# Kernel tuning notes

Hardware: AMD Instinct MI355X
Metric: run time of the kernel (lower is better)

## Reference

```python
import jax, jax.numpy as jnp
from jax import lax
import numpy as np

B, N = 64, 8192


def setup_inputs() -> dict:
    key = jax.random.key(0)
    ks = jax.random.split(key, 8)
    v = jax.random.normal(ks[0], (B, N), jnp.float32)
    mask = (jax.random.uniform(ks[1], (B, N)) > 0.5).astype(jnp.float32)
    def init_w(k, shape, fan_in):
        return (jax.random.normal(k, shape, jnp.float32) / np.float32(np.sqrt(fan_in)))
    # Conv1d weights: (out_ch, in_ch, kernel)
    w1 = init_w(ks[2], (32, 2, 5), 2 * 5)
    b1 = jnp.zeros((32,), jnp.float32)
    w2 = init_w(ks[3], (32, 32, 5), 32 * 5)
    b2 = jnp.zeros((32,), jnp.float32)
    w3 = init_w(ks[4], (2, 32, 5), 32 * 5)
    b3 = jnp.zeros((2,), jnp.float32)
    return dict(v=v, mask=mask, w1=w1, b1=b1, w2=w2, b2=b2, w3=w3, b3=b3)


def _bk_gii(he_diag):
    """Diagonal of G = (zI - H)^{-1} for tridiagonal H (diag=he_diag, sub=super=1), z=1j.
    Uses the standard left/right continued-fraction recursions:
      L_0 = z - a_0,   L_i = z - a_i - 1/L_{i-1}
      R_{N-1} = z - a_{N-1},   R_i = z - a_i - 1/R_{i+1}
      G_ii = 1 / (L_i + R_i - (z - a_i))
    Returns (B, N, 2) features = [Re G_ii, Im G_ii]."""
    z = jnp.complex64(1j)
    a = he_diag.astype(jnp.complex64).T  # (N, B)

    def step(carry, a_i):
        nxt = z - a_i - 1.0 / carry
        return nxt, nxt

    L0 = z - a[0]
    _, Ls = lax.scan(step, L0, a[1:])
    L = jnp.concatenate([L0[None], Ls], axis=0)  # (N, B)

    Rl = z - a[-1]
    _, Rs = lax.scan(step, Rl, a[:-1][::-1])
    R = jnp.concatenate([Rl[None], Rs], axis=0)[::-1]  # (N, B)

    G = 1.0 / (L + R - (z - a))  # (N, B) complex
    return jnp.stack([G.real, G.imag], axis=-1).transpose(1, 0, 2)  # (B, N, 2)


def _conv1d(x, w, b):
    # x: (B, C_in, N), w: (C_out, C_in, K=5), 'same' padding (pad=2)
    y = lax.conv_general_dilated(x, w, window_strides=(1,), padding=[(2, 2)],
                                 dimension_numbers=('NCH', 'OIH', 'NCH'))
    return y + b[None, :, None]


def reference(v, mask, w1, b1, w2, b2, w3, b3):
    he_diag = v - 2.0  # h0_diag_base (-2.0) + v
    feats_full = _bk_gii(he_diag)                 # (B, N, 2)
    feats_sparse = feats_full * mask[..., None]   # zero out unmasked positions
    # learned interpolator: Conv1d(2->32)->ReLU->Conv1d(32->32)->ReLU->Conv1d(32->2)
    x = feats_sparse.transpose(0, 2, 1)           # (B, 2, N)
    x = jax.nn.relu(_conv1d(x, w1, b1))
    x = jax.nn.relu(_conv1d(x, w2, b2))
    feats_interp = _conv1d(x, w3, b3).transpose(0, 2, 1)  # (B, N, 2)
    feats_final = jnp.where(mask[..., None] > 0.5, feats_sparse, feats_interp)
    return feats_final, feats_sparse
```

## Files before the change

kernel.cpp:

```cpp
#include <hip/hip_runtime.h>
#include <hip/hip_bf16.h>


#define BB 64
#define NN 8192
#define KWARM 16
#define TSEG 1024
#define H 8
#define PCH 8
#define NCH 130
#define STG0 320
#define CHK 256
#define NT 512
#define HST 40

using half8  = __attribute__((ext_vector_type(8))) _Float16;
using f32x16 = __attribute__((ext_vector_type(16))) float;

__device__ __forceinline__ half8 ld16(const ushort* p) {
    return *reinterpret_cast<const half8*>(p);
}
__device__ __forceinline__ ushort f2h(float x) {
    _Float16 h = (_Float16)x;
    return __builtin_bit_cast(unsigned short, h);
}
__device__ __forceinline__ uint pk2rn(float a, float b) {
    union { _Float16 h[2]; uint u; } r;
    r.h[0] = (_Float16)a; r.h[1] = (_Float16)b;
    return r.u;
}
__device__ __forceinline__ float h2f(ushort u) {
    return (float)__builtin_bit_cast(_Float16, u);
}

#define CSTV(RV, IV, AV) { float dd_ = RV*RV + IV*IV;                      \
    float iv_ = __builtin_amdgcn_rcpf(dd_);                                \
    float nr_ = -(AV) - RV*iv_;                                            \
    IV = 1.0f + IV*iv_; RV = nr_; }
#define GC(LRV, LIV, RRV, RIV, AV, MM, GR, GI) {                           \
    float Dr_ = LRV + RRV + (AV), Di_ = LIV + RIV - 1.0f;                  \
    float iv_ = __builtin_amdgcn_rcpf(Dr_*Dr_ + Di_*Di_);                  \
    GR = Dr_*iv_*(MM); GI = -Di_*iv_*(MM); }

__global__ __launch_bounds__(NT, 4) void fused_kernel(
    const float* __restrict__ v,  const float* __restrict__ mask,
    const float* __restrict__ w1, const float* __restrict__ b1,
    const float* __restrict__ w2, const float* __restrict__ b2,
    const float* __restrict__ w3, const float* __restrict__ b3,
    float* __restrict__ outF, float* __restrict__ fs)
{
    __shared__ __align__(16) ushort h1t[264 * HST];
    __shared__ __align__(16) ushort h2t[260 * HST];
    __shared__ __align__(16) ushort wt1c[32 * 32];
    __shared__ __align__(16) ushort wt2c[32 * 176];
    __shared__ __align__(16) ushort wt3c[2 * 160];
    __shared__ __align__(16) uint   xsp[TSEG + 2*H + 8];
    __shared__ __align__(8) unsigned char mskb[TSEG];
    __shared__ float b3s[2];

    const int tid  = threadIdx.x;
    const int b    = blockIdx.y;
    const int s    = blockIdx.x * TSEG;
    const int base = s - H - KWARM;

    float* sa = reinterpret_cast<float*>(h1t);

    for (int i = tid; i < TSEG + 2*H + 2*KWARM; i += NT) {
        int g = base + i; g = min(max(g, 0), NN - 1);
        sa[i] = v[b * NN + g] - 2.0f;
    }
    __syncthreads();

    if (tid < NCH) {
        const int e0 = s - H + PCH * tid;
        if (e0 >= 0 && e0 + PCH <= NN) {
            float4 mva = *reinterpret_cast<const float4*>(&mask[b * NN + e0]);
            float4 mvb = *reinterpret_cast<const float4*>(&mask[b * NN + e0 + 4]);
            const float4* s4 = reinterpret_cast<const float4*>(sa);
            float4 aA = s4[2*tid + 4];
            float4 aB = s4[2*tid + 5];
            float Lr, Li, Rr, Ri;
            const bool fast = (e0 - KWARM >= 0) && (e0 + 7 + KWARM <= NN - 1);
            if (fast) {
                float4 cL = s4[2*tid];
                float4 cR = s4[2*tid + 9];
                Lr = -cL.x; Li = 1.0f; Rr = -cR.w; Ri = 1.0f;
                CSTV(Lr, Li, cL.y); CSTV(Rr, Ri, cR.z);
                CSTV(Lr, Li, cL.z); CSTV(Rr, Ri, cR.y);
                CSTV(Lr, Li, cL.w); CSTV(Rr, Ri, cR.x);
                #pragma unroll
                for (int g = 1; g <= 3; ++g) {
                    float4 nL = s4[2*tid + g];
                    float4 nR = s4[2*tid + 9 - g];
                    CSTV(Lr, Li, nL.x); CSTV(Rr, Ri, nR.w);
                    CSTV(Lr, Li, nL.y); CSTV(Rr, Ri, nR.z);
                    CSTV(Lr, Li, nL.z); CSTV(Rr, Ri, nR.y);
                    CSTV(Lr, Li, nL.w); CSTV(Rr, Ri, nR.x);
                }
                CSTV(Lr, Li, aA.x);
                CSTV(Rr, Ri, aB.w);
            } else {
                int j0 = max(e0 - KWARM, 0);
                Lr = -sa[j0 - base]; Li = 1.0f;
                for (int j = j0 + 1; j <= e0; ++j) CSTV(Lr, Li, sa[j - base]);
                int j1 = min(e0 + 7 + KWARM, NN - 1);
                Rr = -sa[j1 - base]; Ri = 1.0f;
                for (int j = j1 - 1; j >= e0 + 7; --j) CSTV(Rr, Ri, sa[j - base]);
            }
            float L0r = Lr, L0i = Li;
            CSTV(Lr, Li, aA.y); float L1r = Lr, L1i = Li;
            CSTV(Lr, Li, aA.z); float L2r = Lr, L2i = Li;
            CSTV(Lr, Li, aA.w); float L3r = Lr, L3i = Li;
            CSTV(Lr, Li, aB.x); float L4r = Lr, L4i = Li;
            CSTV(Lr, Li, aB.y); float L5r = Lr, L5i = Li;
            CSTV(Lr, Li, aB.z); float L6r = Lr, L6i = Li;
            CSTV(Lr, Li, aB.w); float L7r = Lr, L7i = Li;
            float g0r,g0i,g1r,g1i,g2r,g2i,g3r,g3i,g4r,g4i,g5r,g5i,g6r,g6i,g7r,g7i;
            GC(L7r, L7i, Rr, Ri, aB.w, mvb.w, g7r, g7i);
            CSTV(Rr, Ri, aB.z); GC(L6r, L6i, Rr, Ri, aB.z, mvb.z, g6r, g6i);
            CSTV(Rr, Ri, aB.y); GC(L5r, L5i, Rr, Ri, aB.y, mvb.y, g5r, g5i);
            CSTV(Rr, Ri, aB.x); GC(L4r, L4i, Rr, Ri, aB.x, mvb.x, g4r, g4i);
            CSTV(Rr, Ri, aA.w); GC(L3r, L3i, Rr, Ri, aA.w, mva.w, g3r, g3i);
            CSTV(Rr, Ri, aA.z); GC(L2r, L2i, Rr, Ri, aA.z, mva.z, g2r, g2i);
            CSTV(Rr, Ri, aA.y); GC(L1r, L1i, Rr, Ri, aA.y, mva.y, g1r, g1i);
            CSTV(Rr, Ri, aA.x); GC(L0r, L0i, Rr, Ri, aA.x, mva.x, g0r, g0i);

            uint4 pkA, pkB;
            pkA.x = (uint)f2h(g0r) | ((uint)f2h(g0i) << 16);
            pkA.y = (uint)f2h(g1r) | ((uint)f2h(g1i) << 16);
            pkA.z = (uint)f2h(g2r) | ((uint)f2h(g2i) << 16);
            pkA.w = (uint)f2h(g3r) | ((uint)f2h(g3i) << 16);
            pkB.x = (uint)f2h(g4r) | ((uint)f2h(g4i) << 16);
            pkB.y = (uint)f2h(g5r) | ((uint)f2h(g5i) << 16);
            pkB.z = (uint)f2h(g6r) | ((uint)f2h(g6i) << 16);
            pkB.w = (uint)f2h(g7r) | ((uint)f2h(g7i) << 16);
            *reinterpret_cast<uint4*>(&xsp[PCH * tid])     = pkA;
            *reinterpret_cast<uint4*>(&xsp[PCH * tid + 4]) = pkB;

            if (e0 >= s && e0 < s + TSEG) {
                size_t off = ((size_t)b * NN + e0) * 2;
                *reinterpret_cast<float4*>(&fs[off])      = make_float4(g0r, g0i, g1r, g1i);
                *reinterpret_cast<float4*>(&fs[off + 4])  = make_float4(g2r, g2i, g3r, g3i);
                *reinterpret_cast<float4*>(&fs[off + 8])  = make_float4(g4r, g4i, g5r, g5i);
                *reinterpret_cast<float4*>(&fs[off + 12]) = make_float4(g6r, g6i, g7r, g7i);
                uint mb0 = (mva.x > 0.5f ? 1u : 0u) | (mva.y > 0.5f ? 1u : 0u) << 8
                         | (mva.z > 0.5f ? 1u : 0u) << 16 | (mva.w > 0.5f ? 1u : 0u) << 24;
                uint mb1 = (mvb.x > 0.5f ? 1u : 0u) | (mvb.y > 0.5f ? 1u : 0u) << 8
                         | (mvb.z > 0.5f ? 1u : 0u) << 16 | (mvb.w > 0.5f ? 1u : 0u) << 24;
                *reinterpret_cast<uint2*>(&mskb[e0 - s]) = make_uint2(mb0, mb1);
            }
        } else {
            uint4 z = {0u, 0u, 0u, 0u};
            *reinterpret_cast<uint4*>(&xsp[PCH * tid])     = z;
            *reinterpret_cast<uint4*>(&xsp[PCH * tid + 4]) = z;
        }
    } else if (tid < NCH + 8) {
        xsp[TSEG + 2*H + (tid - NCH)] = 0u;
    } else if (tid >= STG0) {
        const int t0 = tid - STG0;
        for (int i = t0; i < 1024; i += 192) {
            int co = i >> 5, k = i & 31;
            ushort val = 0;
            if (k < 10)       val = f2h(w1[co*10 + (k&1)*5 + (k>>1)]);
            else if (k == 10) val = f2h(b1[co]);
            wt1c[i] = val;
        }
        for (int i = t0; i < 5120; i += 192) {
            int co = i / 160, r = i - co*160;
            wt2c[co*176 + (r % 5)*32 + r/5] = f2h(w2[i]);
        }
        for (int i = t0; i < 512; i += 192) {
            int co = i >> 4, k = 160 + (i & 15);
            wt2c[co*176 + k] = (k == 160) ? f2h(b2[co]) : (ushort)0;
        }
        for (int i = t0; i < 320; i += 192) {
            int co = i / 160, r = i - co*160;
            wt3c[co*160 + (r % 5)*32 + r/5] = f2h(w3[i]);
        }
        if (t0 < 2) b3s[t0] = b3[t0];
    }
    __syncthreads();

    const int lane = tid & 63;
    const int wv   = tid >> 6;
    const int cn   = lane & 31;
    const int kh   = lane >> 5;
    const int kh4  = 4 * kh;

    union { half8 v8; uint u[4]; } on;
    on.u[0] = kh ? 0u : 0x3C00u; on.u[1] = 0u; on.u[2] = 0u; on.u[3] = 0u;
    const half8 onesF = on.v8;

    half8 wA1 = ld16(&wt1c[cn * 32 + 8 * kh]);
    half8 wA2[11];
    #pragma unroll
    for (int t = 0; t < 11; ++t) wA2[t] = ld16(&wt2c[cn*176 + 16*t + 8*kh]);
    const float bz0 = b3s[0], bz1 = b3s[1];

    for (int ch = 0; ch < 4; ++ch) {
        const int cr = ch * CHK;

        #pragma unroll
        for (int pass = 0; pass < 2; ++pass) {
            int t = (pass == 0) ? wv : ((wv == 0) ? 8 : -1);
            if (t >= 0) {
                int tb1 = (t < 8) ? 32*t : 232;
                int mi  = cr + 2 + tb1 + cn;
                union { half8 v8; uint u[4]; } B;
                if (kh == 0) { B.u[0]=xsp[mi];   B.u[1]=xsp[mi+1];
                               B.u[2]=xsp[mi+2]; B.u[3]=xsp[mi+3]; }
                else         { B.u[0]=xsp[mi+4]; B.u[1]=0x3C00u;
                               B.u[2]=0; B.u[3]=0; }
                f32x16 a1 = {};
                a1 = __builtin_amdgcn_mfma_f32_32x32x16_f16(wA1, B.v8, a1, 0, 0, 0);
                int row = tb1 + cn;
                int gp  = s + cr - 4 + row;
                bool ok = (gp >= 0) && (gp < NN);
                ushort* rp = &h1t[row * HST + kh4];
                #pragma unroll
                for (int q = 0; q < 4; ++q) {
                    uint lo = pk2rn(fmaxf(a1[4*q+0], 0.f), fmaxf(a1[4*q+1], 0.f));
                    uint hi = pk2rn(fmaxf(a1[4*q+2], 0.f), fmaxf(a1[4*q+3], 0.f));
                    *reinterpret_cast<uint2*>(rp + 8*q) =
                        make_uint2(ok ? lo : 0u, ok ? hi : 0u);
                }
            }
        }
        __syncthreads();

        #pragma unroll
        for (int pass = 0; pass < 2; ++pass) {
            int t = (pass == 0) ? wv : ((wv == 1) ? 8 : -1);
            if (t >= 0) {
                int tb2 = (t < 8) ? 32*t : 228;
                f32x16 acc = {};
                #pragma unroll
                for (int q = 0; q < 10; ++q) {
                    int kidx = 16*q + 8*kh;
                    half8 Bf = ld16(&h1t[(tb2 + cn + (kidx >> 5))*HST + (kidx & 31)]);
                    acc = __builtin_amdgcn_mfma_f32_32x32x16_f16(wA2[q], Bf, acc, 0, 0, 0);
                }
                acc = __builtin_amdgcn_mfma_f32_32x32x16_f16(wA2[10], onesF, acc, 0, 0, 0);
                int row = tb2 + cn;
                int gp  = s + cr - 2 + row;
                bool ok = (gp >= 0) && (gp < NN);
                ushort* rp = &h2t[row * HST + kh4];
                #pragma unroll
                for (int q = 0; q < 4; ++q) {
                    uint lo = pk2rn(fmaxf(acc[4*q+0], 0.f), fmaxf(acc[4*q+1], 0.f));
                    uint hi = pk2rn(fmaxf(acc[4*q+2], 0.f), fmaxf(acc[4*q+3], 0.f));
                    *reinterpret_cast<uint2*>(rp + 8*q) =
                        make_uint2(ok ? lo : 0u, ok ? hi : 0u);
                }
            }
        }
        __syncthreads();

        {
            const int tb3 = 32 * wv;
            f32x16 a3 = {};
            half8 z = {};
            const int wb = ((cn < 2) ? cn : 0) * 160;
            #pragma unroll
            for (int q = 0; q < 10; ++q) {
                int kidx = 16*q + 8*kh;
                half8 Af = (cn < 2) ? ld16(&wt3c[wb + 16*q + 8*kh]) : z;
                half8 Bf = ld16(&h2t[(tb3 + cn + (kidx >> 5))*HST + (kidx & 31)]);
                a3 = __builtin_amdgcn_mfma_f32_32x32x16_f16(Af, Bf, a3, 0, 0, 0);
            }
            if (kh == 0) {
                int p = cr + tb3 + cn;
                uint xp = xsp[H + p];
                bool m  = mskb[p] != 0;
                float ox = m ? h2f((ushort)(xp & 0xffffu)) : (a3[0] + bz0);
                float oy = m ? h2f((ushort)(xp >> 16))     : (a3[1] + bz1);
                *reinterpret_cast<float2*>(&outF[((size_t)b*NN + s + p)*2]) =
                    make_float2(ox, oy);
            }
        }
    }
}

extern "C" void kernel_launch(void* const* d_in, const int* in_sizes, int n_in,
                              void* d_out, int out_size, void* d_ws, size_t ws_size,
                              hipStream_t stream) {
    const float* v    = (const float*)d_in[0];
    const float* mask = (const float*)d_in[1];
    const float* w1   = (const float*)d_in[2];
    const float* b1   = (const float*)d_in[3];
    const float* w2   = (const float*)d_in[4];
    const float* b2   = (const float*)d_in[5];
    const float* w3   = (const float*)d_in[6];
    const float* b3   = (const float*)d_in[7];

    float* outF = (float*)d_out;
    float* fs   = outF + (size_t)BB * NN * 2;

    dim3 g(NN / TSEG, BB);
    fused_kernel<<<g, NT, 0, stream>>>(v, mask, w1, b1, w2, b2, w3, b3, outF, fs);
}
```

Before: 24.31 us.

## Carry conv halo rows across chunks to drop extra conv1/conv2 tiles

```diff
diff --git a/kernel.cpp b/kernel.cpp
--- a/kernel.cpp
+++ b/kernel.cpp
@@ -16,6 +16,8 @@
 
 using half8  = __attribute__((ext_vector_type(8))) _Float16;
 using f32x16 = __attribute__((ext_vector_type(16))) float;
+
+#define FENCE() asm volatile("" ::: "memory")
 
 __device__ __forceinline__ half8 ld16(const ushort* p) {
     return *reinterpret_cast<const half8*>(p);
@@ -197,62 +199,71 @@
     for (int t = 0; t < 11; ++t) wA2[t] = ld16(&wt2c[cn*176 + 16*t + 8*kh]);
     const float bz0 = b3s[0], bz1 = b3s[1];
 
+    auto conv1_tile = [&](int cr, int tb1) {
+        int mi = cr + 2 + tb1 + cn;
+        union { half8 v8; uint u[4]; } B;
+        if (kh == 0) { B.u[0]=xsp[mi];   B.u[1]=xsp[mi+1];
+                       B.u[2]=xsp[mi+2]; B.u[3]=xsp[mi+3]; }
+        else         { B.u[0]=xsp[mi+4]; B.u[1]=0x3C00u;
+                       B.u[2]=0; B.u[3]=0; }
+        f32x16 a1 = {};
+        a1 = __builtin_amdgcn_mfma_f32_32x32x16_f16(wA1, B.v8, a1, 0, 0, 0);
+        int row = tb1 + cn;
+        int gp  = s + cr - 4 + row;
+        bool ok = (gp >= 0) && (gp < NN);
+        ushort* rp = &h1t[row * HST + kh4];
+        #pragma unroll
+        for (int q = 0; q < 4; ++q) {
+            uint lo = pk2rn(fmaxf(a1[4*q+0], 0.f), fmaxf(a1[4*q+1], 0.f));
+            uint hi = pk2rn(fmaxf(a1[4*q+2], 0.f), fmaxf(a1[4*q+3], 0.f));
+            *reinterpret_cast<uint2*>(rp + 8*q) =
+                make_uint2(ok ? lo : 0u, ok ? hi : 0u);
+        }
+    };
+    auto conv2_tile = [&](int cr, int tb2) {
+        f32x16 acc = {};
+        #pragma unroll
+        for (int q = 0; q < 10; ++q) {
+            int kidx = 16*q + 8*kh;
+            half8 Bf = ld16(&h1t[(tb2 + cn + (kidx >> 5))*HST + (kidx & 31)]);
+            acc = __builtin_amdgcn_mfma_f32_32x32x16_f16(wA2[q], Bf, acc, 0, 0, 0);
+        }
+        acc = __builtin_amdgcn_mfma_f32_32x32x16_f16(wA2[10], onesF, acc, 0, 0, 0);
+        int row = tb2 + cn;
+        int gp  = s + cr - 2 + row;
+        bool ok = (gp >= 0) && (gp < NN);
+        ushort* rp = &h2t[row * HST + kh4];
+        #pragma unroll
+        for (int q = 0; q < 4; ++q) {
+            uint lo = pk2rn(fmaxf(acc[4*q+0], 0.f), fmaxf(acc[4*q+1], 0.f));
+            uint hi = pk2rn(fmaxf(acc[4*q+2], 0.f), fmaxf(acc[4*q+3], 0.f));
+            *reinterpret_cast<uint2*>(rp + 8*q) =
+                make_uint2(ok ? lo : 0u, ok ? hi : 0u);
+        }
+    };
+
     for (int ch = 0; ch < 4; ++ch) {
         const int cr = ch * CHK;
 
-        #pragma unroll
-        for (int pass = 0; pass < 2; ++pass) {
-            int t = (pass == 0) ? wv : ((wv == 0) ? 8 : -1);
-            if (t >= 0) {
-                int tb1 = (t < 8) ? 32*t : 232;
-                int mi  = cr + 2 + tb1 + cn;
-                union { half8 v8; uint u[4]; } B;
-                if (kh == 0) { B.u[0]=xsp[mi];   B.u[1]=xsp[mi+1];
-                               B.u[2]=xsp[mi+2]; B.u[3]=xsp[mi+3]; }
-                else         { B.u[0]=xsp[mi+4]; B.u[1]=0x3C00u;
-                               B.u[2]=0; B.u[3]=0; }
-                f32x16 a1 = {};
-                a1 = __builtin_amdgcn_mfma_f32_32x32x16_f16(wA1, B.v8, a1, 0, 0, 0);
-                int row = tb1 + cn;
-                int gp  = s + cr - 4 + row;
-                bool ok = (gp >= 0) && (gp < NN);
-                ushort* rp = &h1t[row * HST + kh4];
-                #pragma unroll
-                for (int q = 0; q < 4; ++q) {
-                    uint lo = pk2rn(fmaxf(a1[4*q+0], 0.f), fmaxf(a1[4*q+1], 0.f));
-                    uint hi = pk2rn(fmaxf(a1[4*q+2], 0.f), fmaxf(a1[4*q+3], 0.f));
-                    *reinterpret_cast<uint2*>(rp + 8*q) =
-                        make_uint2(ok ? lo : 0u, ok ? hi : 0u);
-                }
-            }
+        if (ch == 0) {
+            conv1_tile(cr, 32 * wv);
+            if (wv == 0) conv1_tile(cr, 232);
+        } else {
+            conv1_tile(cr, 8 + 32 * wv);
         }
         __syncthreads();
 
-        #pragma unroll
-        for (int pass = 0; pass < 2; ++pass) {
-            int t = (pass == 0) ? wv : ((wv == 1) ? 8 : -1);
-            if (t >= 0) {
-                int tb2 = (t < 8) ? 32*t : 228;
-                f32x16 acc = {};
-                #pragma unroll
-                for (int q = 0; q < 10; ++q) {
-                    int kidx = 16*q + 8*kh;
-                    half8 Bf = ld16(&h1t[(tb2 + cn + (kidx >> 5))*HST + (kidx & 31)]);
-                    acc = __builtin_amdgcn_mfma_f32_32x32x16_f16(wA2[q], Bf, acc, 0, 0, 0);
-                }
-                acc = __builtin_amdgcn_mfma_f32_32x32x16_f16(wA2[10], onesF, acc, 0, 0, 0);
-                int row = tb2 + cn;
-                int gp  = s + cr - 2 + row;
-                bool ok = (gp >= 0) && (gp < NN);
-                ushort* rp = &h2t[row * HST + kh4];
-                #pragma unroll
-                for (int q = 0; q < 4; ++q) {
-                    uint lo = pk2rn(fmaxf(acc[4*q+0], 0.f), fmaxf(acc[4*q+1], 0.f));
-                    uint hi = pk2rn(fmaxf(acc[4*q+2], 0.f), fmaxf(acc[4*q+3], 0.f));
-                    *reinterpret_cast<uint2*>(rp + 8*q) =
-                        make_uint2(ok ? lo : 0u, ok ? hi : 0u);
-                }
-            }
+        if (ch == 0) {
+            conv2_tile(cr, 32 * wv);
+            if (wv == 1) conv2_tile(cr, 228);
+        } else {
+            conv2_tile(cr, 4 + 32 * wv);
+        }
+        if (ch < 3 && wv == 0 && lane < 40) {
+            FENCE();
+            int r = lane / 10, q = lane % 10;
+            *reinterpret_cast<uint2*>(&h1t[(4 + r)*HST + 4*q]) =
+                *reinterpret_cast<const uint2*>(&h1t[(260 + r)*HST + 4*q]);
         }
         __syncthreads();
 
@@ -278,6 +289,12 @@
                     make_float2(ox, oy);
             }
         }
+        if (ch < 3 && wv == 0 && lane < 40) {
+            FENCE();
+            int r = lane / 10, q = lane % 10;
+            *reinterpret_cast<uint2*>(&h2t[r*HST + 4*q]) =
+                *reinterpret_cast<const uint2*>(&h2t[(256 + r)*HST + 4*q]);
+        }
     }
 }
 
```

Result: no change. 23.99 us (-1.3%).
